# Optimization experiments

Measured on AMD Instinct MI355X. Metric: run time of the kernel, lower is better.

Reference implementation:

```python
import jax, jax.numpy as jnp
import numpy as np

N_COMP = 36          # sdf_n_comp
GRID = 300           # gridSize per axis
SDF_DIM = 256
APP_DIM = 128
MULTIRES = 3         # sdf positional-encoding octaves -> 3 + 3*2*3 = 21 channels
N_PTS = 524288       # sample points per batch (~1024 rays x 512 samples)
EMB_CH = 3 + 3 * 2 * MULTIRES            # 21
IN_CH = EMB_CH + 3 * N_COMP              # 129
OUT_CH = 1 + APP_DIM                     # 129 (sdf + appearance feature)
INIT_RADIUS = 0.2


def setup_inputs() -> dict:
    key = jax.random.key(0)
    ks = jax.random.split(key, 6)
    xyz_sampled = jax.random.uniform(ks[0], (N_PTS, 3), jnp.float32) * 2.0 - 1.0
    # tensor-decomposition grids (stacked over the 3 VM planes)
    planes = jax.random.normal(ks[1], (3, N_COMP, GRID, GRID), jnp.float32) * 0.1
    lines = jax.random.normal(ks[2], (3, N_COMP, GRID), jnp.float32) * (1.0 / (N_COMP * 3))
    # sdf_mat MLP params, initialized per init_mlp()
    w1 = jax.random.normal(ks[3], (SDF_DIM, IN_CH), jnp.float32) * (np.sqrt(2.0) / np.sqrt(SDF_DIM))
    b1 = jnp.zeros((SDF_DIM,), jnp.float32)
    w2 = jax.random.normal(ks[4], (OUT_CH, SDF_DIM), jnp.float32) * 1e-4 + np.sqrt(np.pi) / np.sqrt(SDF_DIM)
    b2 = jnp.full((OUT_CH,), -INIT_RADIUS, jnp.float32)
    return {"xyz_sampled": xyz_sampled, "planes": planes, "lines": lines,
            "w1": w1, "b1": b1, "w2": w2, "b2": b2}


def _bilin2d(plane, x, y):
    """Bilinear grid_sample, align_corners=True. plane [C,H,W]; x,y [N] in [-1,1] -> [C,N]."""
    C, H, W = plane.shape
    fx = (x + 1.0) * 0.5 * (W - 1)
    fy = (y + 1.0) * 0.5 * (H - 1)
    x0 = jnp.clip(jnp.floor(fx).astype(jnp.int32), 0, W - 2)
    y0 = jnp.clip(jnp.floor(fy).astype(jnp.int32), 0, H - 2)
    tx = fx - x0
    ty = fy - y0
    v00 = plane[:, y0, x0]
    v01 = plane[:, y0, x0 + 1]
    v10 = plane[:, y0 + 1, x0]
    v11 = plane[:, y0 + 1, x0 + 1]
    return (v00 * (1 - tx) * (1 - ty) + v01 * tx * (1 - ty)
            + v10 * (1 - tx) * ty + v11 * tx * ty)


def _lin1d(line, z):
    """Linear grid_sample, align_corners=True. line [C,L]; z [N] in [-1,1] -> [C,N]."""
    C, L = line.shape
    fz = (z + 1.0) * 0.5 * (L - 1)
    z0 = jnp.clip(jnp.floor(fz).astype(jnp.int32), 0, L - 2)
    tz = fz - z0
    return line[:, z0] * (1 - tz) + line[:, z0 + 1] * tz


def _embed(x):
    """NeRF positional encoding, include_input, octaves 2^0..2^(MULTIRES-1). [N,3] -> [N,21]."""
    freqs = 2.0 ** jnp.arange(MULTIRES, dtype=x.dtype)
    ang = x[:, :, None] * freqs  # [N,3,MULTIRES]
    n = x.shape[0]
    return jnp.concatenate([x, jnp.sin(ang).reshape(n, -1), jnp.cos(ang).reshape(n, -1)], axis=-1)


def reference(xyz_sampled, planes, lines, w1, b1, w2, b2):
    # aabb = [-1,1]^3 -> normalization is identity, kept explicit for faithfulness
    xn = (xyz_sampled - (-1.0)) / 2.0 * 2.0 - 1.0
    # matMode=[[0,1],[0,2],[1,2]], vecMode=[2,1,0]
    px = jnp.stack([xn[:, 0], xn[:, 0], xn[:, 1]])  # [3,N] first plane coord
    py = jnp.stack([xn[:, 1], xn[:, 2], xn[:, 2]])  # [3,N] second plane coord
    pz = jnp.stack([xn[:, 2], xn[:, 1], xn[:, 0]])  # [3,N] line coord
    pf = jax.vmap(_bilin2d)(planes, px, py)         # [3,C,N]
    lf = jax.vmap(_lin1d)(lines, pz)                # [3,C,N]
    feat = (pf * lf).transpose(2, 0, 1).reshape(xn.shape[0], -1)  # [N, 3*C]
    mlp_in = jnp.concatenate([_embed(xyz_sampled), feat], axis=-1)  # [N, 129]
    h = jax.nn.softplus(100.0 * (mlp_in @ w1.T + b1)) / 100.0       # Softplus(beta=100)
    out = h @ w2.T + b2                                             # [N, 1+app_dim]
    return out
```

## Files before the change

### kernel.cpp

```cpp
#include <hip/hip_runtime.h>
#include <hip/hip_bf16.h>
#include <cstdint>
#include <cstddef>


using half2v = __attribute__((ext_vector_type(2))) _Float16;
using half4  = __attribute__((ext_vector_type(4))) _Float16;
using half8  = __attribute__((ext_vector_type(8))) _Float16;
using floatx4 = __attribute__((ext_vector_type(4))) float;

#define NPTS    524288
#define GRES    300
#define NCOMP   36
#define SDFD    256
#define IN_CH   129
#define IN_PAD  160
#define OUT_CH  129
#define OUT_PAD 144
#define TILE_M  64
#define S_IN    168
#define S_H     264

#define OFF_W1S 0
#define SZ_W1S  (5*4*256*8*2)
#define OFF_W2S (OFF_W1S + SZ_W1S)
#define SZ_W2S  (8*4*144*8*2)
#define OFF_PLT (OFF_W2S + SZ_W2S)
#define SZ_PLT  (3*300*300*36*2)
#define OFF_LT  (OFF_PLT + SZ_PLT)
#define SZ_LT   (3*300*36*2)
#define WS_NEED_FAST ((size_t)(OFF_LT + SZ_LT))


__global__ void prep_planes_k(const float* __restrict__ planes, _Float16* __restrict__ pl_t) {
    int idx = blockIdx.x * 256 + threadIdx.x;
    if (idx >= 3 * GRES * GRES) return;
    int x = idx % GRES; int t = idx / GRES; int y = t % GRES; int m = t / GRES;
    _Float16* dst = pl_t + (size_t)idx * NCOMP;
    const float* src = planes + (size_t)m * NCOMP * GRES * GRES + (size_t)y * GRES + x;
    #pragma unroll
    for (int c4 = 0; c4 < NCOMP; c4 += 4) {
        half4 o;
        #pragma unroll
        for (int i = 0; i < 4; ++i)
            o[i] = (_Float16)src[(size_t)(c4 + i) * GRES * GRES];
        *(half4*)(dst + c4) = o;
    }
}

#define NB_W1 ((5*4*256*8 + 255)/256)
#define NB_W2 ((8*4*144*8 + 255)/256)
#define NB_L  ((3*GRES + 255)/256)
__global__ void prep_small_k(const float* __restrict__ w1, const float* __restrict__ w2,
                             const float* __restrict__ lines,
                             _Float16* __restrict__ w1s, _Float16* __restrict__ w2s,
                             _Float16* __restrict__ l_t) {
    int b = blockIdx.x;
    if (b < NB_W1) {
        int t = b * 256 + threadIdx.x;
        if (t >= 5 * 4 * 256 * 8) return;
        int j = t & 7; int n = (t >> 3) & 255; int q = t >> 11;
        int k = (q >> 2) * 32 + (q & 3) * 8 + j;
        float v = 0.f;
        if (k < IN_CH) {
            int ko = (k < 108) ? (21 + k) : (k - 108);
            v = w1[n * IN_CH + ko];
        }
        w1s[t] = (_Float16)v;
    } else if (b < NB_W1 + NB_W2) {
        int t = (b - NB_W1) * 256 + threadIdx.x;
        if (t >= 8 * 4 * 144 * 8) return;
        int j = t & 7; int r = t >> 3; int n = r % 144; int q = r / 144;
        int k = (q >> 2) * 32 + (q & 3) * 8 + j;
        float v = (n < OUT_CH) ? w2[n * SDFD + k] : 0.f;
        w2s[t] = (_Float16)v;
    } else {
        int idx = (b - NB_W1 - NB_W2) * 256 + threadIdx.x;
        if (idx >= 3 * GRES) return;
        int z = idx % GRES; int m = idx / GRES;
        _Float16* dst = l_t + (size_t)idx * NCOMP;
        const float* src = lines + ((size_t)m * NCOMP) * GRES + z;
        for (int c = 0; c < NCOMP; ++c)
            dst[c] = (_Float16)src[(size_t)c * GRES];
    }
}


__device__ __forceinline__ float softplus100(float z) {
    return fmaxf(z, 0.f) + __logf(1.f + __expf(-fabsf(z)));
}

template <bool FAST>
__global__ __launch_bounds__(256, 2)
void tsdf_fused_k(const float* __restrict__ xyz,
                  const float* __restrict__ planes,
                  const float* __restrict__ lines,
                  const _Float16* __restrict__ pl_t,
                  const _Float16* __restrict__ l_t,
                  const _Float16* __restrict__ w1s,
                  const _Float16* __restrict__ w2s,
                  const float* __restrict__ b1,
                  const float* __restrict__ b2,
                  float* __restrict__ out)
{
    __shared__ _Float16 mlp_lds[TILE_M * S_IN];
    __shared__ _Float16 h_lds[TILE_M * S_H];
    const int tid = threadIdx.x;
    const int blk = blockIdx.x;

    {
        const int p   = tid >> 2;
        const int sub = tid & 3;
        const size_t gp = (size_t)blk * TILE_M + p;
        const float X = xyz[gp * 3 + 0];
        const float Y = xyz[gp * 3 + 1];
        const float Z = xyz[gp * 3 + 2];
        if (sub < 3) {
            const int m = sub;
            const float px = (m == 2) ? Y : X;
            const float py = (m == 0) ? Y : Z;
            const float pz = (m == 0) ? Z : ((m == 1) ? Y : X);
            float fx = (px + 1.f) * 0.5f * 299.f;
            float fy = (py + 1.f) * 0.5f * 299.f;
            float fz = (pz + 1.f) * 0.5f * 299.f;
            int x0 = (int)floorf(fx); x0 = x0 < 0 ? 0 : (x0 > 298 ? 298 : x0);
            int y0 = (int)floorf(fy); y0 = y0 < 0 ? 0 : (y0 > 298 ? 298 : y0);
            int z0 = (int)floorf(fz); z0 = z0 < 0 ? 0 : (z0 > 298 ? 298 : z0);
            const float tx = fx - (float)x0, ty = fy - (float)y0, tz = fz - (float)z0;
            const float w00 = (1.f - tx) * (1.f - ty), w01 = tx * (1.f - ty);
            const float w10 = (1.f - tx) * ty,         w11 = tx * ty;
            const float lw0 = 1.f - tz, lw1 = tz;
            _Float16* dst = &mlp_lds[p * S_IN + m * NCOMP];
            if (FAST) {
                const _Float16 h00 = (_Float16)w00, h01 = (_Float16)w01;
                const _Float16 h10 = (_Float16)w10, h11 = (_Float16)w11;
                const _Float16 hl0 = (_Float16)lw0, hl1 = (_Float16)lw1;
                const half4 W00 = {h00, h00, h00, h00}, W01 = {h01, h01, h01, h01};
                const half4 W10 = {h10, h10, h10, h10}, W11 = {h11, h11, h11, h11};
                const half4 WL0 = {hl0, hl0, hl0, hl0}, WL1 = {hl1, hl1, hl1, hl1};
                const _Float16* b00 = pl_t + ((size_t)(m * GRES + y0) * GRES + x0) * NCOMP;
                const _Float16* lb  = l_t + (size_t)(m * GRES + z0) * NCOMP;
                #pragma unroll
                for (int c = 0; c < NCOMP; c += 4) {
                    half4 v00 = *(const half4*)(b00 + c);
                    half4 v01 = *(const half4*)(b00 + NCOMP + c);
                    half4 v10 = *(const half4*)(b00 + GRES * NCOMP + c);
                    half4 v11 = *(const half4*)(b00 + GRES * NCOMP + NCOMP + c);
                    half4 l0  = *(const half4*)(lb + c);
                    half4 l1  = *(const half4*)(lb + NCOMP + c);
                    half4 pf = v00 * W00 + v01 * W01 + v10 * W10 + v11 * W11;
                    half4 lf = l0 * WL0 + l1 * WL1;
                    *(half4*)(dst + c) = pf * lf;
                }
            } else {
                const float* pb = planes + (size_t)m * NCOMP * GRES * GRES;
                for (int c = 0; c < NCOMP; ++c) {
                    const float* pc = pb + (size_t)c * GRES * GRES + (size_t)y0 * GRES + x0;
                    const float* lc = lines + ((size_t)m * NCOMP + c) * GRES + z0;
                    float pf = pc[0] * w00 + pc[1] * w01 + pc[GRES] * w10 + pc[GRES + 1] * w11;
                    float lf = lc[0] * lw0 + lc[1] * lw1;
                    dst[c] = (_Float16)(pf * lf);
                }
            }
        } else {
            _Float16* e = &mlp_lds[p * S_IN];
            e[108] = (_Float16)X; e[109] = (_Float16)Y; e[110] = (_Float16)Z;
            const float v3[3] = {X, Y, Z};
            #pragma unroll
            for (int d = 0; d < 3; ++d) {
                float f = 1.f;
                #pragma unroll
                for (int q = 0; q < 3; ++q) {
                    const float a = v3[d] * f;
                    e[111 + d * 3 + q] = (_Float16)__sinf(a);
                    e[120 + d * 3 + q] = (_Float16)__cosf(a);
                    f *= 2.f;
                }
            }
            e[129] = (_Float16)0.f;
            #pragma unroll
            for (int k = 130; k < IN_PAD; k += 2)
                *(half2v*)&e[k] = (half2v){(_Float16)0.f, (_Float16)0.f};
        }
    }
    __syncthreads();

    const int lane = tid & 63;
    const int wv   = tid >> 6;
    const int l15  = lane & 15;
    const int quad = lane >> 4;

    floatx4 acc1[4][4];
    #pragma unroll
    for (int mt = 0; mt < 4; ++mt)
        #pragma unroll
        for (int nt = 0; nt < 4; ++nt)
            acc1[mt][nt] = (floatx4){0.f, 0.f, 0.f, 0.f};

    #pragma unroll
    for (int s = 0; s < 5; ++s) {
        half8 a[4], b[4];
        #pragma unroll
        for (int mt = 0; mt < 4; ++mt)
            a[mt] = *(const half8*)&mlp_lds[(mt * 16 + l15) * S_IN + s * 32 + quad * 8];
        #pragma unroll
        for (int nt = 0; nt < 4; ++nt)
            b[nt] = *(const half8*)&w1s[((size_t)(s * 4 + quad) * 256 + wv * 64 + nt * 16 + l15) * 8];
        #pragma unroll
        for (int mt = 0; mt < 4; ++mt)
            #pragma unroll
            for (int nt = 0; nt < 4; ++nt)
                acc1[mt][nt] = __builtin_amdgcn_mfma_f32_16x16x32_f16(a[mt], b[nt], acc1[mt][nt], 0, 0, 0);
    }
    #pragma unroll
    for (int nt = 0; nt < 4; ++nt) {
        const int n = wv * 64 + nt * 16 + l15;
        const float bias = b1[n];
        #pragma unroll
        for (int mt = 0; mt < 4; ++mt) {
            #pragma unroll
            for (int r = 0; r < 4; ++r) {
                const float z = 100.f * (acc1[mt][nt][r] + bias);
                h_lds[(mt * 16 + quad * 4 + r) * S_H + n] = (_Float16)(softplus100(z) * 0.01f);
            }
        }
    }
    __syncthreads();

    floatx4 acc2[9];
    #pragma unroll
    for (int nt = 0; nt < 9; ++nt) acc2[nt] = (floatx4){0.f, 0.f, 0.f, 0.f};

    #pragma unroll
    for (int s = 0; s < 8; ++s) {
        const half8 a = *(const half8*)&h_lds[(wv * 16 + l15) * S_H + s * 32 + quad * 8];
        #pragma unroll
        for (int nt = 0; nt < 9; ++nt) {
            const half8 b = *(const half8*)&w2s[((size_t)(s * 4 + quad) * 144 + nt * 16 + l15) * 8];
            acc2[nt] = __builtin_amdgcn_mfma_f32_16x16x32_f16(a, b, acc2[nt], 0, 0, 0);
        }
    }
    const int m_lo = wv * 16 + quad * 4;
    #pragma unroll
    for (int nt = 0; nt < 9; ++nt) {
        const int n = nt * 16 + l15;
        if (n < OUT_CH) {
            const float bias = b2[n];
            #pragma unroll
            for (int r = 0; r < 4; ++r) {
                const size_t gm = (size_t)blk * TILE_M + m_lo + r;
                out[gm * OUT_CH + n] = acc2[nt][r] + bias;
            }
        }
    }
}


extern "C" void kernel_launch(void* const* d_in, const int* in_sizes, int n_in,
                              void* d_out, int out_size, void* d_ws, size_t ws_size,
                              hipStream_t stream) {
    const float* xyz    = (const float*)d_in[0];
    const float* planes = (const float*)d_in[1];
    const float* lines  = (const float*)d_in[2];
    const float* w1     = (const float*)d_in[3];
    const float* b1     = (const float*)d_in[4];
    const float* w2     = (const float*)d_in[5];
    const float* b2     = (const float*)d_in[6];
    float* out = (float*)d_out;
    char* ws = (char*)d_ws;

    _Float16* w1s  = (_Float16*)(ws + OFF_W1S);
    _Float16* w2s  = (_Float16*)(ws + OFF_W2S);
    _Float16* pl_t = (_Float16*)(ws + OFF_PLT);
    _Float16* l_t  = (_Float16*)(ws + OFF_LT);

    const bool fast = (ws_size >= WS_NEED_FAST);

    prep_small_k<<<NB_W1 + NB_W2 + NB_L, 256, 0, stream>>>(w1, w2, lines, w1s, w2s, l_t);

    if (fast) {
        prep_planes_k<<<(3 * GRES * GRES + 255) / 256, 256, 0, stream>>>(planes, pl_t);
        tsdf_fused_k<true><<<NPTS / TILE_M, 256, 0, stream>>>(
            xyz, planes, lines, pl_t, l_t, w1s, w2s, b1, b2, out);
    } else {
        tsdf_fused_k<false><<<NPTS / TILE_M, 256, 0, stream>>>(
            xyz, planes, lines, pl_t, l_t, w1s, w2s, b1, b2, out);
    }
}
```

Baseline: 581.4 us.

## Alias LDS buffers, swizzle hidden tile, retile layer-2 GEMM, merge prep kernels

The MLP input tile and hidden-activation tile now share one 32 KB LDS buffer, with an added barrier so layer-1 reads finish before the hidden tile overwrites them. This frees LDS so the launch bound can rise from 2 to 4 blocks per CU. The hidden tile uses an XOR-swizzled layout to avoid bank conflicts. Layer 2 is retiled so each wave covers all 64 rows and reuses each weight fragment across four MFMAs, at the cost of uneven work: wave 0 gets three output tiles, the others two. The plane transpose is merged with the weight and line prep into one kernel and uses an LDS staging buffer for coalesced access; the slow path now also runs this prep, which writes the plane buffer regardless of workspace size.

```diff
diff --git a/kernel.cpp b/kernel.cpp
--- a/kernel.cpp
+++ b/kernel.cpp
@@ -16,10 +16,8 @@
 #define IN_CH   129
 #define IN_PAD  160
 #define OUT_CH  129
-#define OUT_PAD 144
 #define TILE_M  64
 #define S_IN    168
-#define S_H     264
 
 #define OFF_W1S 0
 #define SZ_W1S  (5*4*256*8*2)
@@ -31,33 +29,44 @@
 #define SZ_LT   (3*300*36*2)
 #define WS_NEED_FAST ((size_t)(OFF_LT + SZ_LT))
 
-
-__global__ void prep_planes_k(const float* __restrict__ planes, _Float16* __restrict__ pl_t) {
-    int idx = blockIdx.x * 256 + threadIdx.x;
-    if (idx >= 3 * GRES * GRES) return;
-    int x = idx % GRES; int t = idx / GRES; int y = t % GRES; int m = t / GRES;
-    _Float16* dst = pl_t + (size_t)idx * NCOMP;
-    const float* src = planes + (size_t)m * NCOMP * GRES * GRES + (size_t)y * GRES + x;
-    #pragma unroll
-    for (int c4 = 0; c4 < NCOMP; c4 += 4) {
-        half4 o;
-        #pragma unroll
-        for (int i = 0; i < 4; ++i)
-            o[i] = (_Float16)src[(size_t)(c4 + i) * GRES * GRES];
-        *(half4*)(dst + c4) = o;
-    }
-}
-
+#define NB_PL (3*GRES*5)
 #define NB_W1 ((5*4*256*8 + 255)/256)
 #define NB_W2 ((8*4*144*8 + 255)/256)
 #define NB_L  ((3*GRES + 255)/256)
-__global__ void prep_small_k(const float* __restrict__ w1, const float* __restrict__ w2,
-                             const float* __restrict__ lines,
-                             _Float16* __restrict__ w1s, _Float16* __restrict__ w2s,
-                             _Float16* __restrict__ l_t) {
-    int b = blockIdx.x;
-    if (b < NB_W1) {
-        int t = b * 256 + threadIdx.x;
+
+__global__ __launch_bounds__(256)
+void prep_all_k(const float* __restrict__ planes, const float* __restrict__ lines,
+                const float* __restrict__ w1, const float* __restrict__ w2,
+                _Float16* __restrict__ pl_t, _Float16* __restrict__ l_t,
+                _Float16* __restrict__ w1s, _Float16* __restrict__ w2s) {
+    const int b = blockIdx.x;
+    const int tid = threadIdx.x;
+    if (b < NB_PL) {
+        __shared__ float lbuf[NCOMP][65];
+        const int m  = b / (GRES * 5);
+        const int r0 = b % (GRES * 5);
+        const int y  = r0 / 5;
+        const int x0 = (r0 % 5) * 64;
+        const int W  = (x0 + 64 <= GRES) ? 64 : (GRES - x0);
+        const float* src = planes + (size_t)m * NCOMP * GRES * GRES + (size_t)y * GRES + x0;
+        #pragma unroll
+        for (int e = tid; e < NCOMP * 64; e += 256) {
+            const int c = e >> 6, x = e & 63;
+            if (x < W) lbuf[c][x] = src[(size_t)c * GRES * GRES + x];
+        }
+        __syncthreads();
+        _Float16* dst = pl_t + ((size_t)(m * GRES + y) * GRES + x0) * NCOMP;
+        #pragma unroll
+        for (int e = tid; e < 64 * (NCOMP / 2); e += 256) {
+            const int x = e / (NCOMP / 2);
+            const int cc = (e % (NCOMP / 2)) * 2;
+            if (x < W) {
+                half2v o = { (_Float16)lbuf[cc][x], (_Float16)lbuf[cc + 1][x] };
+                *(half2v*)(dst + (size_t)x * NCOMP + cc) = o;
+            }
+        }
+    } else if (b < NB_PL + NB_W1) {
+        int t = (b - NB_PL) * 256 + tid;
         if (t >= 5 * 4 * 256 * 8) return;
         int j = t & 7; int n = (t >> 3) & 255; int q = t >> 11;
         int k = (q >> 2) * 32 + (q & 3) * 8 + j;
@@ -67,15 +76,15 @@
             v = w1[n * IN_CH + ko];
         }
         w1s[t] = (_Float16)v;
-    } else if (b < NB_W1 + NB_W2) {
-        int t = (b - NB_W1) * 256 + threadIdx.x;
+    } else if (b < NB_PL + NB_W1 + NB_W2) {
+        int t = (b - NB_PL - NB_W1) * 256 + tid;
         if (t >= 8 * 4 * 144 * 8) return;
         int j = t & 7; int r = t >> 3; int n = r % 144; int q = r / 144;
         int k = (q >> 2) * 32 + (q & 3) * 8 + j;
         float v = (n < OUT_CH) ? w2[n * SDFD + k] : 0.f;
         w2s[t] = (_Float16)v;
     } else {
-        int idx = (b - NB_W1 - NB_W2) * 256 + threadIdx.x;
+        int idx = (b - NB_PL - NB_W1 - NB_W2) * 256 + tid;
         if (idx >= 3 * GRES) return;
         int z = idx % GRES; int m = idx / GRES;
         _Float16* dst = l_t + (size_t)idx * NCOMP;
@@ -90,8 +99,15 @@
     return fmaxf(z, 0.f) + __logf(1.f + __expf(-fabsf(z)));
 }
 
+__device__ __forceinline__ int h_idx(int row, int col) {
+    return row * 256 + ((((col >> 3) ^ (row & 7)) << 3) | (col & 7));
+}
+__device__ __forceinline__ int h_idx8(int row, int chunk) {
+    return row * 256 + ((chunk ^ (row & 7)) << 3);
+}
+
 template <bool FAST>
-__global__ __launch_bounds__(256, 2)
+__global__ __launch_bounds__(256, 4)
 void tsdf_fused_k(const float* __restrict__ xyz,
                   const float* __restrict__ planes,
                   const float* __restrict__ lines,
@@ -103,8 +119,9 @@
                   const float* __restrict__ b2,
                   float* __restrict__ out)
 {
-    __shared__ _Float16 mlp_lds[TILE_M * S_IN];
-    __shared__ _Float16 h_lds[TILE_M * S_H];
+    __shared__ __align__(16) _Float16 u_lds[16384];
+    _Float16* mlp_lds = u_lds;
+    _Float16* h_lds   = u_lds;
     const int tid = threadIdx.x;
     const int blk = blockIdx.x;
 
@@ -129,12 +146,11 @@
             const float tx = fx - (float)x0, ty = fy - (float)y0, tz = fz - (float)z0;
             const float w00 = (1.f - tx) * (1.f - ty), w01 = tx * (1.f - ty);
             const float w10 = (1.f - tx) * ty,         w11 = tx * ty;
-            const float lw0 = 1.f - tz, lw1 = tz;
             _Float16* dst = &mlp_lds[p * S_IN + m * NCOMP];
             if (FAST) {
                 const _Float16 h00 = (_Float16)w00, h01 = (_Float16)w01;
                 const _Float16 h10 = (_Float16)w10, h11 = (_Float16)w11;
-                const _Float16 hl0 = (_Float16)lw0, hl1 = (_Float16)lw1;
+                const _Float16 hl0 = (_Float16)(1.f - tz), hl1 = (_Float16)tz;
                 const half4 W00 = {h00, h00, h00, h00}, W01 = {h01, h01, h01, h01};
                 const half4 W10 = {h10, h10, h10, h10}, W11 = {h11, h11, h11, h11};
                 const half4 WL0 = {hl0, hl0, hl0, hl0}, WL1 = {hl1, hl1, hl1, hl1};
@@ -153,6 +169,7 @@
                     *(half4*)(dst + c) = pf * lf;
                 }
             } else {
+                const float lw0 = 1.f - tz, lw1 = tz;
                 const float* pb = planes + (size_t)m * NCOMP * GRES * GRES;
                 for (int c = 0; c < NCOMP; ++c) {
                     const float* pc = pb + (size_t)c * GRES * GRES + (size_t)y0 * GRES + x0;
@@ -212,6 +229,8 @@
             for (int nt = 0; nt < 4; ++nt)
                 acc1[mt][nt] = __builtin_amdgcn_mfma_f32_16x16x32_f16(a[mt], b[nt], acc1[mt][nt], 0, 0, 0);
     }
+    __syncthreads();
+
     #pragma unroll
     for (int nt = 0; nt < 4; ++nt) {
         const int n = wv * 64 + nt * 16 + l15;
@@ -221,35 +240,51 @@
             #pragma unroll
             for (int r = 0; r < 4; ++r) {
                 const float z = 100.f * (acc1[mt][nt][r] + bias);
-                h_lds[(mt * 16 + quad * 4 + r) * S_H + n] = (_Float16)(softplus100(z) * 0.01f);
+                h_lds[h_idx(mt * 16 + quad * 4 + r, n)] = (_Float16)(softplus100(z) * 0.01f);
             }
         }
     }
     __syncthreads();
 
-    floatx4 acc2[9];
-    #pragma unroll
-    for (int nt = 0; nt < 9; ++nt) acc2[nt] = (floatx4){0.f, 0.f, 0.f, 0.f};
+    const int nnt = (wv == 0) ? 3 : 2;
+    floatx4 acc2[3][4];
+    #pragma unroll
+    for (int i = 0; i < 3; ++i)
+        #pragma unroll
+        for (int mt = 0; mt < 4; ++mt)
+            acc2[i][mt] = (floatx4){0.f, 0.f, 0.f, 0.f};
 
     #pragma unroll
     for (int s = 0; s < 8; ++s) {
-        const half8 a = *(const half8*)&h_lds[(wv * 16 + l15) * S_H + s * 32 + quad * 8];
-        #pragma unroll
-        for (int nt = 0; nt < 9; ++nt) {
-            const half8 b = *(const half8*)&w2s[((size_t)(s * 4 + quad) * 144 + nt * 16 + l15) * 8];
-            acc2[nt] = __builtin_amdgcn_mfma_f32_16x16x32_f16(a, b, acc2[nt], 0, 0, 0);
-        }
-    }
-    const int m_lo = wv * 16 + quad * 4;
-    #pragma unroll
-    for (int nt = 0; nt < 9; ++nt) {
-        const int n = nt * 16 + l15;
-        if (n < OUT_CH) {
-            const float bias = b2[n];
-            #pragma unroll
-            for (int r = 0; r < 4; ++r) {
-                const size_t gm = (size_t)blk * TILE_M + m_lo + r;
-                out[gm * OUT_CH + n] = acc2[nt][r] + bias;
+        half8 a[4];
+        #pragma unroll
+        for (int mt = 0; mt < 4; ++mt)
+            a[mt] = *(const half8*)&h_lds[h_idx8(mt * 16 + l15, s * 4 + quad)];
+        #pragma unroll
+        for (int i = 0; i < 3; ++i) {
+            if (i < nnt) {
+                const int nt = wv + i * 4;
+                const half8 b = *(const half8*)&w2s[((size_t)(s * 4 + quad) * 144 + nt * 16 + l15) * 8];
+                #pragma unroll
+                for (int mt = 0; mt < 4; ++mt)
+                    acc2[i][mt] = __builtin_amdgcn_mfma_f32_16x16x32_f16(a[mt], b, acc2[i][mt], 0, 0, 0);
+            }
+        }
+    }
+    #pragma unroll
+    for (int i = 0; i < 3; ++i) {
+        if (i < nnt) {
+            const int n = (wv + i * 4) * 16 + l15;
+            if (n < OUT_CH) {
+                const float bias = b2[n];
+                #pragma unroll
+                for (int mt = 0; mt < 4; ++mt) {
+                    #pragma unroll
+                    for (int r = 0; r < 4; ++r) {
+                        const size_t gm = (size_t)blk * TILE_M + mt * 16 + quad * 4 + r;
+                        out[gm * OUT_CH + n] = acc2[i][mt][r] + bias;
+                    }
+                }
             }
         }
     }
@@ -276,13 +311,14 @@
 
     const bool fast = (ws_size >= WS_NEED_FAST);
 
-    prep_small_k<<<NB_W1 + NB_W2 + NB_L, 256, 0, stream>>>(w1, w2, lines, w1s, w2s, l_t);
-
     if (fast) {
-        prep_planes_k<<<(3 * GRES * GRES + 255) / 256, 256, 0, stream>>>(planes, pl_t);
+        prep_all_k<<<NB_PL + NB_W1 + NB_W2 + NB_L, 256, 0, stream>>>(
+            planes, lines, w1, w2, pl_t, l_t, w1s, w2s);
         tsdf_fused_k<true><<<NPTS / TILE_M, 256, 0, stream>>>(
             xyz, planes, lines, pl_t, l_t, w1s, w2s, b1, b2, out);
     } else {
+        prep_all_k<<<NB_PL + NB_W1 + NB_W2 + NB_L, 256, 0, stream>>>(
+            planes, lines, w1, w2, pl_t, l_t, w1s, w2s);
         tsdf_fused_k<false><<<NPTS / TILE_M, 256, 0, stream>>>(
             xyz, planes, lines, pl_t, l_t, w1s, w2s, b1, b2, out);
     }
```

Measured after the change: 613.9 us. 5.6% more time.
